# Kernel tuning notes

Measured on AMD Instinct MI355X. Metric: run time of the kernel, lower is better.

## Reference

```python
import jax, jax.numpy as jnp
import numpy as np

D = 1280      # embed_dim
H = 20        # num_heads
HD = D // H   # head_dim = 64
B = 4         # batch (number of requests)
ENC = 1500    # encoder length per request (Whisper 30s)
KV = B * ENC  # 6000 packed cross kv tokens
SEQ = [300, 500, 350, 450]  # ragged decoder lengths, sum = 1600
Q = sum(SEQ)


def setup_inputs() -> dict:
    key = jax.random.key(0)
    ks = jax.random.split(key, 8)
    s = 0.02
    return {
        "hidden_states": jax.random.normal(ks[0], (Q, D), jnp.float32),
        "cross_hidden_states": jax.random.normal(ks[1], (KV, D), jnp.float32),
        "seq_lens": jnp.array(SEQ, dtype=jnp.int32),
        "Wq": jax.random.normal(ks[2], (D, D), jnp.float32) * s,
        "bq": jax.random.normal(ks[3], (D,), jnp.float32) * s,
        "Wkv": jax.random.normal(ks[4], (D, 2 * D), jnp.float32) * s,
        "bkv": jax.random.normal(ks[5], (2 * D,), jnp.float32) * s,
        "Wo": jax.random.normal(ks[6], (D, D), jnp.float32) * s,
        "bo": jax.random.normal(ks[7], (D,), jnp.float32) * s,
    }


def reference(hidden_states, cross_hidden_states, seq_lens, Wq, bq, Wkv, bkv, Wo, bo):
    q_len, d = hidden_states.shape
    kv_len = cross_hidden_states.shape[0]
    bsz = seq_lens.shape[0]
    enc_len = kv_len // bsz
    scaling = jnp.float32(HD) ** -0.5

    # projections (packed tokens)
    q = (hidden_states @ Wq + bq) * scaling           # [Q, D]
    kv = cross_hidden_states @ Wkv + bkv              # [KV, 2D]
    k, v = kv[:, :d], kv[:, d:]

    # [H, L, HD]
    qh = q.reshape(q_len, H, HD).transpose(1, 0, 2)
    kh = k.reshape(kv_len, H, HD).transpose(1, 0, 2)
    vh = v.reshape(kv_len, H, HD).transpose(1, 0, 2)

    scores = jnp.einsum("hqd,hkd->hqk", qh, kh)       # [H, Q, KV]

    # ragged block-diagonal mask: query token i belongs to request
    # searchsorted(cumsum(seq_lens), i, 'right'); kv token j to j // enc_len
    cum = jnp.cumsum(seq_lens)
    q_req = jnp.searchsorted(cum, jnp.arange(q_len), side="right")
    kv_req = jnp.arange(kv_len) // enc_len
    mask = q_req[:, None] == kv_req[None, :]          # [Q, KV] bool

    scores = jnp.where(mask[None, :, :], scores, -jnp.inf)
    probs = jax.nn.softmax(scores, axis=-1)
    attn = jnp.einsum("hqk,hkd->hqd", probs, vh)      # [H, Q, HD]
    attn = attn.transpose(1, 0, 2).reshape(q_len, d)
    return attn @ Wo + bo
```

## Files before the change

### kernel.cpp

```cpp
#include <hip/hip_runtime.h>
#include <stdint.h>

#define AS1 __attribute__((address_space(1)))
#define AS3 __attribute__((address_space(3)))

typedef __bf16 bf16_t;
typedef bf16_t bf16x8 __attribute__((ext_vector_type(8)));
typedef float  f32x4  __attribute__((ext_vector_type(4)));
typedef float  f32x16 __attribute__((ext_vector_type(16)));
typedef unsigned short u16;

constexpr int D     = 1280;
constexpr int H     = 20;
constexpr int HD    = 64;
constexpr int NQ    = 1600;
constexpr int NKV   = 6000;
constexpr int ENC   = 1500;
constexpr int QPAD  = 1632;
constexpr int KVP   = 1504;
constexpr int KVTOT = 4 * KVP;
constexpr int KB_PER_REQ = KVP / 32;
constexpr int KB_TOT     = 4 * KB_PER_REQ;

__device__ __forceinline__ u16 f2bf(float f) {
  union { float f; uint32_t u; } x; x.f = f;
  uint32_t r = (x.u + 0x7fffu + ((x.u >> 16) & 1u)) >> 16;
  return (u16)r;
}

__device__ __forceinline__ void gload16(const void* g, void* l) {
  __builtin_amdgcn_global_load_lds((AS1 void*)g, (AS3 void*)l, 16, 0, 0);
}

__device__ __forceinline__ void cvt_body(const float* __restrict__ in, u16* __restrict__ out,
                                         int i, int n4) {
  if (i >= n4) return;
  float4 v = ((const float4*)in)[i];
  ushort4 o;
  o.x = f2bf(v.x); o.y = f2bf(v.y); o.z = f2bf(v.z); o.w = f2bf(v.w);
  ((ushort4*)out)[i] = o;
}

__device__ __forceinline__ void tpose_body(const float* __restrict__ in, u16* __restrict__ out,
                                           int R, int C, int bx, int by, u16 (*tile)[33]) {
  int bc = bx * 32, br = by * 32;
  int tx = threadIdx.x & 31, ty = threadIdx.x >> 5;
#pragma unroll
  for (int i = 0; i < 32; i += 8)
    tile[ty + i][tx] = f2bf(in[(size_t)(br + ty + i) * C + bc + tx]);
  __syncthreads();
#pragma unroll
  for (int i = 0; i < 32; i += 8)
    out[(size_t)(bc + ty + i) * R + br + tx] = tile[tx][ty + i];
}

__global__ __launch_bounds__(256)
void prep_kernel(const float* __restrict__ hs, const float* __restrict__ chs,
                 const float* __restrict__ Wq, const float* __restrict__ Wkv,
                 const float* __restrict__ Wo,
                 u16* __restrict__ hsb, u16* __restrict__ chsb,
                 u16* __restrict__ Wqt, u16* __restrict__ Wkvt, u16* __restrict__ Wot) {
  __shared__ u16 tile[32][33];
  int b = blockIdx.x;
  if (b < 2000) {
    cvt_body(hs, hsb, b * 256 + threadIdx.x, 512000);
  } else if (b < 9500) {
    cvt_body(chs, chsb, (b - 2000) * 256 + threadIdx.x, 1920000);
  } else if (b < 11100) {
    int t = b - 9500;  tpose_body(Wq,  Wqt,  1280, 1280, t % 40, t / 40, tile);
  } else if (b < 14300) {
    int t = b - 11100; tpose_body(Wkv, Wkvt, 1280, 2560, t % 80, t / 80, tile);
  } else {
    int t = b - 14300; tpose_body(Wo,  Wot,  1280, 1280, t % 40, t / 40, tile);
  }
}

template <int MODE>
__device__ __forceinline__ void gemm_tile(
    int m0, int n0, const u16* __restrict__ A, const u16* __restrict__ Bt,
    const float* __restrict__ bias, int M,
    u16* __restrict__ outA, u16* __restrict__ outB, float* __restrict__ outF,
    u16* As, u16* Bs) {
  const int tid = threadIdx.x;
  const int lane = tid & 63, l15 = lane & 15, lg = lane >> 4;
  const int w = tid >> 6, wr = w >> 1, wc = w & 1;

  const bool vside = (MODE == 1) && (n0 >= D);

  f32x4 acc[4][4] = {};

  for (int k0 = 0; k0 < D; k0 += 64) {
#pragma unroll
    for (int p = 0; p < 4; ++p) {
      int off = p * 4096 + tid * 16;
      int lg_off = off ^ (((off >> 7) & 7) << 4);
      int row = lg_off >> 7, kb = lg_off & 127;
      int gr = m0 + row; gr = gr < M ? gr : M - 1;
      gload16((const char*)A + ((size_t)gr * D + k0) * 2 + kb, (char*)As + off);
    }
#pragma unroll
    for (int p = 0; p < 4; ++p) {
      int off = p * 4096 + tid * 16;
      int lg_off = off ^ (((off >> 7) & 7) << 4);
      int row = lg_off >> 7, kb = lg_off & 127;
      int gr = n0 + row;
      gload16((const char*)Bt + ((size_t)gr * D + k0) * 2 + kb, (char*)Bs + off);
    }
    __syncthreads();
#pragma unroll
    for (int kk = 0; kk < 2; ++kk) {
      const int kbyte = kk * 64 + lg * 16;
      bf16x8 af[4], bfr[4];
#pragma unroll
      for (int m = 0; m < 4; ++m) {
        int row = wr * 64 + m * 16 + l15;
        int addr = ((row << 7) + kbyte) ^ ((row & 7) << 4);
        af[m] = *(const bf16x8*)((const char*)As + addr);
      }
#pragma unroll
      for (int n = 0; n < 4; ++n) {
        int row = wc * 64 + n * 16 + l15;
        int addr = ((row << 7) + kbyte) ^ ((row & 7) << 4);
        bfr[n] = *(const bf16x8*)((const char*)Bs + addr);
      }
      if (!vside) {
#pragma unroll
        for (int m = 0; m < 4; ++m)
#pragma unroll
          for (int n = 0; n < 4; ++n)
            acc[m][n] = __builtin_amdgcn_mfma_f32_16x16x32_bf16(af[m], bfr[n], acc[m][n], 0, 0, 0);
      } else {
#pragma unroll
        for (int m = 0; m < 4; ++m)
#pragma unroll
          for (int n = 0; n < 4; ++n)
            acc[m][n] = __builtin_amdgcn_mfma_f32_16x16x32_bf16(bfr[n], af[m], acc[m][n], 0, 0, 0);
      }
    }
    __syncthreads();
  }

  if (!vside) {
#pragma unroll
    for (int m = 0; m < 4; ++m)
#pragma unroll
      for (int n = 0; n < 4; ++n) {
        int col = n0 + wc * 64 + n * 16 + l15;
        float bv = bias[col];
#pragma unroll
        for (int r = 0; r < 4; ++r) {
          int row = m0 + wr * 64 + m * 16 + lg * 4 + r;
          if (row >= M) continue;
          float v = acc[m][n][r] + bv;
          if (MODE == 0) {
            v *= 0.125f;
            int h = col >> 6, hd = col & 63;
            outA[((size_t)(h * QPAD + row)) * HD + hd] = f2bf(v);
          } else {
            int req = row / ENC, loc = row - req * ENC;
            int rr = req * KVP + loc;
            int h = col >> 6, hd = col & 63;
            int kb2 = rr >> 5, kv = rr & 31;
            outA[((size_t)((h * KB_TOT + kb2) * 4 + (hd >> 4))) * 512 + kv * 16 + (hd & 15)] = f2bf(v);
          }
        }
      }
  } else {
    float bvv[4][4];
#pragma unroll
    for (int n = 0; n < 4; ++n)
#pragma unroll
      for (int r = 0; r < 4; ++r)
        bvv[n][r] = bias[n0 + wc * 64 + n * 16 + lg * 4 + r];
#pragma unroll
    for (int m = 0; m < 4; ++m) {
      int gm = m0 + wr * 64 + m * 16 + l15;
      int req = gm / ENC, loc = gm - req * ENC;
      int rr = req * KVP + loc;
      int kb2 = rr >> 5, kv = rr & 31;
      bool ok = gm < M;
#pragma unroll
      for (int n = 0; n < 4; ++n)
#pragma unroll
        for (int r = 0; r < 4; ++r) {
          if (!ok) continue;
          int c2 = n0 + wc * 64 + n * 16 + lg * 4 + r - D;
          int h = c2 >> 6, hd = c2 & 63;
          outB[((size_t)((h * KB_TOT + kb2) * 64 + hd)) * 32 + kv] = f2bf(acc[m][n][r] + bvv[n][r]);
        }
    }
  }
}

__global__ __launch_bounds__(256)
void qkv_gemm_kernel(const u16* __restrict__ hsb, const u16* __restrict__ chsb,
                     const u16* __restrict__ Wqt, const u16* __restrict__ Wkvt,
                     const float* __restrict__ bq, const float* __restrict__ bkv,
                     u16* __restrict__ qhb, u16* __restrict__ khb, u16* __restrict__ vtb) {
  __shared__ __align__(16) u16 As[128 * 64];
  __shared__ __align__(16) u16 Bs[128 * 64];
  const int bid = blockIdx.x;
  if (bid < 940) {
    const int q8 = 940 >> 3, r8 = 940 & 7;
    const int xcd = bid & 7, pos = bid >> 3;
    const int wg = (xcd < r8 ? xcd * (q8 + 1) : r8 * (q8 + 1) + (xcd - r8) * q8) + pos;
    gemm_tile<1>((wg / 20) * 128, (wg % 20) * 128, chsb, Wkvt, bkv, NKV,
                 khb, vtb, nullptr, As, Bs);
  } else {
    const int b2 = bid - 940;
    const int q8 = 130 >> 3, r8 = 130 & 7;
    const int xcd = b2 & 7, pos = b2 >> 3;
    const int wg = (xcd < r8 ? xcd * (q8 + 1) : r8 * (q8 + 1) + (xcd - r8) * q8) + pos;
    gemm_tile<0>((wg / 10) * 128, (wg % 10) * 128, hsb, Wqt, bq, NQ,
                 qhb, nullptr, nullptr, As, Bs);
  }
}

__global__ __launch_bounds__(256)
void o_gemm_kernel(const u16* __restrict__ attnb, const u16* __restrict__ Wot,
                   const float* __restrict__ bo, float* __restrict__ out) {
  __shared__ __align__(16) u16 As[128 * 64];
  __shared__ __align__(16) u16 Bs[64 * 64];
  const int nwg = 260, q8 = nwg >> 3, r8 = nwg & 7;
  const int xcd = blockIdx.x & 7, pos = blockIdx.x >> 3;
  const int wg = (xcd < r8 ? xcd * (q8 + 1) : r8 * (q8 + 1) + (xcd - r8) * q8) + pos;
  const int m0 = (wg / 20) * 128, n0 = (wg % 20) * 64;

  const int tid = threadIdx.x;
  const int lane = tid & 63, l15 = lane & 15, lg = lane >> 4;
  const int w = tid >> 6, wr = w >> 1, wc = w & 1;

  f32x4 acc[4][2] = {};

  for (int k0 = 0; k0 < D; k0 += 64) {
#pragma unroll
    for (int p = 0; p < 4; ++p) {
      int off = p * 4096 + tid * 16;
      int lg_off = off ^ (((off >> 7) & 7) << 4);
      int row = lg_off >> 7, kb = lg_off & 127;
      int gr = m0 + row; gr = gr < NQ ? gr : NQ - 1;
      gload16((const char*)attnb + ((size_t)gr * D + k0) * 2 + kb, (char*)As + off);
    }
#pragma unroll
    for (int p = 0; p < 2; ++p) {
      int off = p * 4096 + tid * 16;
      int lg_off = off ^ (((off >> 7) & 7) << 4);
      int row = lg_off >> 7, kb = lg_off & 127;
      gload16((const char*)Wot + ((size_t)(n0 + row) * D + k0) * 2 + kb, (char*)Bs + off);
    }
    __syncthreads();
#pragma unroll
    for (int kk = 0; kk < 2; ++kk) {
      const int kbyte = kk * 64 + lg * 16;
      bf16x8 af[4], bfr[2];
#pragma unroll
      for (int m = 0; m < 4; ++m) {
        int row = wr * 64 + m * 16 + l15;
        int addr = ((row << 7) + kbyte) ^ ((row & 7) << 4);
        af[m] = *(const bf16x8*)((const char*)As + addr);
      }
#pragma unroll
      for (int n = 0; n < 2; ++n) {
        int row = wc * 32 + n * 16 + l15;
        int addr = ((row << 7) + kbyte) ^ ((row & 7) << 4);
        bfr[n] = *(const bf16x8*)((const char*)Bs + addr);
      }
#pragma unroll
      for (int m = 0; m < 4; ++m)
#pragma unroll
        for (int n = 0; n < 2; ++n)
          acc[m][n] = __builtin_amdgcn_mfma_f32_16x16x32_bf16(af[m], bfr[n], acc[m][n], 0, 0, 0);
    }
    __syncthreads();
  }

#pragma unroll
  for (int m = 0; m < 4; ++m)
#pragma unroll
    for (int n = 0; n < 2; ++n) {
      int col = n0 + wc * 32 + n * 16 + l15;
      float bv = bo[col];
#pragma unroll
      for (int r = 0; r < 4; ++r) {
        int row = m0 + wr * 64 + m * 16 + lg * 4 + r;
        if (row >= NQ) continue;
        out[(size_t)row * D + col] = acc[m][n][r] + bv;
      }
    }
}

__global__ __launch_bounds__(256)
void attn_kernel(const u16* __restrict__ kbuf, const u16* __restrict__ vbuf,
                 const u16* __restrict__ qh, const int* __restrict__ seq,
                 u16* __restrict__ attnb) {
  __shared__ __align__(16) float smem[4][2176];
  const int lane = threadIdx.x & 63;
  const int l31 = lane & 31, h5 = lane >> 5;
  const int w = threadIdx.x >> 6;

  const int xcd = blockIdx.x & 7, pos = blockIdx.x >> 3;
  const int g = xcd * 160 + pos;
  const int p = g >> 4, t = g & 15;
  const int head = p >> 2, req = p & 3;

  int s0 = seq[0], s1 = seq[1], s2 = seq[2];
  int qstart = (req > 0 ? s0 : 0) + (req > 1 ? s1 : 0) + (req > 2 ? s2 : 0);
  int slen = seq[req];
  int q0 = t * 32;
  if (q0 >= slen) return;

  const u16* qrow = qh + ((size_t)(head * QPAD + qstart + q0 + l31)) * HD + h5 * 8;
  bf16x8 qb[4];
#pragma unroll
  for (int ks = 0; ks < 4; ++ks) qb[ks] = *(const bf16x8*)(qrow + ks * 16);

  const u16* kpan = kbuf + (size_t)(head * KB_TOT + req * KB_PER_REQ) * 2048 + l31 * 16 + h5 * 8;
  const u16* vpan = vbuf + (size_t)(head * KB_TOT + req * KB_PER_REQ) * 2048 + l31 * 32 + h5 * 8;
  const float C = 1.44269504088896340736f;
  const float KC = 16.0f * C;

  f32x16 o0 = {}, o1 = {};
  float ls = 0.f;

  const int kvs = w * 384;
  const int kve = (w == 3) ? ENC : kvs + 384;

  bf16x8 kA[4], vA[2][2], kB[4], vB[2][2];

  auto loadKV = [&](bf16x8 (&kk)[4], bf16x8 (&vv)[2][2], int blk) {
    const u16* kp = kpan + (size_t)blk * 2048;
    const u16* vp = vpan + (size_t)blk * 2048;
#pragma unroll
    for (int ks = 0; ks < 4; ++ks) kk[ks] = *(const bf16x8*)(kp + ks * 512);
#pragma unroll
    for (int dt = 0; dt < 2; ++dt)
#pragma unroll
      for (int ks = 0; ks < 2; ++ks)
        vv[dt][ks] = *(const bf16x8*)(vp + dt * 1024 + ks * 16);
  };

  auto step = [&](const bf16x8 (&kk)[4], const bf16x8 (&vv)[2][2], int kvb2, bool mask) {
    f32x16 sa = {};
    __builtin_amdgcn_s_setprio(1);
#pragma unroll
    for (int ks = 0; ks < 4; ++ks)
      sa = __builtin_amdgcn_mfma_f32_32x32x16_bf16(kk[ks], qb[ks], sa, 0, 0, 0);
    __builtin_amdgcn_s_setprio(0);

    if (mask) {
#pragma unroll
      for (int r = 0; r < 16; ++r) {
        int kvr = (r & 3) + 4 * h5 + 8 * (r >> 2);
        sa[r] = (kvb2 + kvr >= ENC) ? -__builtin_inff() : sa[r];
      }
    }

    float psum = 0.f;
#pragma unroll
    for (int r = 0; r < 16; ++r) { sa[r] = exp2f(fmaf(sa[r], C, -KC)); psum += sa[r]; }
    ls += psum;

    uint32_t a[8], x[8];
#pragma unroll
    for (int i = 0; i < 8; ++i) {
      union { bf16_t b[2]; uint32_t u; } tpk;
      tpk.b[0] = (bf16_t)sa[2 * i];
      tpk.b[1] = (bf16_t)sa[2 * i + 1];
      a[i] = tpk.u;
    }
#pragma unroll
    for (int i = 0; i < 8; ++i) x[i] = (uint32_t)__shfl_xor((int)a[i], 32);
    union { uint32_t w4[4]; bf16x8 v; } pb0, pb1;
    pb0.w4[0] = h5 ? x[2] : a[0]; pb0.w4[1] = h5 ? x[3] : a[1];
    pb0.w4[2] = h5 ? a[2] : x[0]; pb0.w4[3] = h5 ? a[3] : x[1];
    pb1.w4[0] = h5 ? x[6] : a[4]; pb1.w4[1] = h5 ? x[7] : a[5];
    pb1.w4[2] = h5 ? a[6] : x[4]; pb1.w4[3] = h5 ? a[7] : x[5];

    __builtin_amdgcn_s_setprio(1);
    o0 = __builtin_amdgcn_mfma_f32_32x32x16_bf16(vv[0][0], pb0.v, o0, 0, 0, 0);
    o0 = __builtin_amdgcn_mfma_f32_32x32x16_bf16(vv[0][1], pb1.v, o0, 0, 0, 0);
    o1 = __builtin_amdgcn_mfma_f32_32x32x16_bf16(vv[1][0], pb0.v, o1, 0, 0, 0);
    o1 = __builtin_amdgcn_mfma_f32_32x32x16_bf16(vv[1][1], pb1.v, o1, 0, 0, 0);
    __builtin_amdgcn_s_setprio(0);
  };

  loadKV(kA, vA, kvs >> 5);
  int kvb = kvs;
  while (kvb + 64 <= kve) {
    loadKV(kB, vB, (kvb + 32) >> 5);
    step(kA, vA, kvb, false);
    int nxt = kvb + 64;
    loadKV(kA, vA, (nxt < kve ? nxt : kvs) >> 5);
    step(kB, vB, kvb + 32, false);
    kvb += 64;
  }
  if (kvb < kve)
    step(kA, vA, kvb, true);

  ls += __shfl_xor(ls, 32);

#pragma unroll
  for (int r = 0; r < 16; ++r) {
    int drow = (r & 3) + 8 * (r >> 2) + 4 * h5;
    smem[w][drow * 33 + l31] = o0[r];
    smem[w][(drow + 32) * 33 + l31] = o1[r];
  }
  if (h5 == 0) smem[w][2144 + l31] = ls;
  __syncthreads();

#pragma unroll
  for (int it = 0; it < 8; ++it) {
    int item = threadIdx.x + it * 256;
    int q = item >> 6, d = item & 63;
    float L = smem[0][2144 + q] + smem[1][2144 + q] +
              smem[2][2144 + q] + smem[3][2144 + q];
    float O = smem[0][d * 33 + q] + smem[1][d * 33 + q] +
              smem[2][d * 33 + q] + smem[3][d * 33 + q];
    int qr = q0 + q;
    if (qr < slen)
      attnb[(size_t)(qstart + qr) * D + head * HD + d] = f2bf(O / L);
  }
}

extern "C" void kernel_launch(void* const* d_in, const int* in_sizes, int n_in,
                              void* d_out, int out_size, void* d_ws, size_t ws_size,
                              hipStream_t stream) {
  const float* hs  = (const float*)d_in[0];
  const float* chs = (const float*)d_in[1];
  const int*   seq = (const int*)d_in[2];
  const float* Wq  = (const float*)d_in[3];
  const float* bq  = (const float*)d_in[4];
  const float* Wkv = (const float*)d_in[5];
  const float* bkv = (const float*)d_in[6];
  const float* Wo  = (const float*)d_in[7];
  const float* bo  = (const float*)d_in[8];

  char* ws = (char*)d_ws;
  u16* hsb   = (u16*)(ws + 0);
  u16* chsb  = (u16*)(ws + 4096000);
  u16* Wqt   = (u16*)(ws + 19456000);
  u16* Wkvt  = (u16*)(ws + 22732800);
  u16* Wot   = (u16*)(ws + 29286400);
  u16* qhb   = (u16*)(ws + 32563200);
  u16* khb   = (u16*)(ws + 36741120);
  u16* vtb   = (u16*)(ws + 52142080);
  u16* attnb = (u16*)(ws + 67543040);

  prep_kernel<<<15900, 256, 0, stream>>>(hs, chs, Wq, Wkv, Wo, hsb, chsb, Wqt, Wkvt, Wot);
  qkv_gemm_kernel<<<1070, 256, 0, stream>>>(hsb, chsb, Wqt, Wkvt, bq, bkv, qhb, khb, vtb);
  attn_kernel<<<1280, 256, 0, stream>>>(khb, vtb, qhb, seq, attnb);
  o_gemm_kernel<<<260, 256, 0, stream>>>(attnb, Wot, bo, (float*)d_out);
}
```

Before: 157.4 us.

## Raise attention kernel occupancy by halving LDS and dropping register double-buffering

```diff
diff --git a/kernel.cpp b/kernel.cpp
--- a/kernel.cpp
+++ b/kernel.cpp
@@ -289,11 +289,11 @@
     }
 }
 
-__global__ __launch_bounds__(256)
+__global__ __launch_bounds__(256, 4)
 void attn_kernel(const u16* __restrict__ kbuf, const u16* __restrict__ vbuf,
                  const u16* __restrict__ qh, const int* __restrict__ seq,
                  u16* __restrict__ attnb) {
-  __shared__ __align__(16) float smem[4][2176];
+  __shared__ __align__(16) float smem[4][1088];
   const int lane = threadIdx.x & 63;
   const int l31 = lane & 31, h5 = lane >> 5;
   const int w = threadIdx.x >> 6;
@@ -325,11 +325,10 @@
   const int kvs = w * 384;
   const int kve = (w == 3) ? ENC : kvs + 384;
 
-  bf16x8 kA[4], vA[2][2], kB[4], vB[2][2];
-
-  auto loadKV = [&](bf16x8 (&kk)[4], bf16x8 (&vv)[2][2], int blk) {
-    const u16* kp = kpan + (size_t)blk * 2048;
-    const u16* vp = vpan + (size_t)blk * 2048;
+  auto step = [&](int kvb2, bool mask) {
+    const u16* kp = kpan + (size_t)(kvb2 >> 5) * 2048;
+    const u16* vp = vpan + (size_t)(kvb2 >> 5) * 2048;
+    bf16x8 kk[4], vv[2][2];
 #pragma unroll
     for (int ks = 0; ks < 4; ++ks) kk[ks] = *(const bf16x8*)(kp + ks * 512);
 #pragma unroll
@@ -337,9 +336,7 @@
 #pragma unroll
       for (int ks = 0; ks < 2; ++ks)
         vv[dt][ks] = *(const bf16x8*)(vp + dt * 1024 + ks * 16);
-  };
-
-  auto step = [&](const bf16x8 (&kk)[4], const bf16x8 (&vv)[2][2], int kvb2, bool mask) {
+
     f32x16 sa = {};
     __builtin_amdgcn_s_setprio(1);
 #pragma unroll
@@ -384,41 +381,35 @@
     __builtin_amdgcn_s_setprio(0);
   };
 
-  loadKV(kA, vA, kvs >> 5);
   int kvb = kvs;
-  while (kvb + 64 <= kve) {
-    loadKV(kB, vB, (kvb + 32) >> 5);
-    step(kA, vA, kvb, false);
-    int nxt = kvb + 64;
-    loadKV(kA, vA, (nxt < kve ? nxt : kvs) >> 5);
-    step(kB, vB, kvb + 32, false);
-    kvb += 64;
-  }
-  if (kvb < kve)
-    step(kA, vA, kvb, true);
+  for (; kvb + 32 <= kve; kvb += 32) step(kvb, false);
+  if (kvb < kve) step(kvb, true);
 
   ls += __shfl_xor(ls, 32);
 
 #pragma unroll
-  for (int r = 0; r < 16; ++r) {
-    int drow = (r & 3) + 8 * (r >> 2) + 4 * h5;
-    smem[w][drow * 33 + l31] = o0[r];
-    smem[w][(drow + 32) * 33 + l31] = o1[r];
-  }
-  if (h5 == 0) smem[w][2144 + l31] = ls;
-  __syncthreads();
-
-#pragma unroll
-  for (int it = 0; it < 8; ++it) {
-    int item = threadIdx.x + it * 256;
-    int q = item >> 6, d = item & 63;
-    float L = smem[0][2144 + q] + smem[1][2144 + q] +
-              smem[2][2144 + q] + smem[3][2144 + q];
-    float O = smem[0][d * 33 + q] + smem[1][d * 33 + q] +
-              smem[2][d * 33 + q] + smem[3][d * 33 + q];
-    int qr = q0 + q;
-    if (qr < slen)
-      attnb[(size_t)(qstart + qr) * D + head * HD + d] = f2bf(O / L);
+  for (int pass = 0; pass < 2; ++pass) {
+    if (pass) __syncthreads();
+#pragma unroll
+    for (int r = 0; r < 16; ++r) {
+      int drow = (r & 3) + 8 * (r >> 2) + 4 * h5;
+      smem[w][drow * 33 + l31] = pass ? o1[r] : o0[r];
+    }
+    if (pass == 0 && h5 == 0) smem[w][1056 + l31] = ls;
+    __syncthreads();
+
+#pragma unroll
+    for (int it = 0; it < 4; ++it) {
+      int item = threadIdx.x + it * 256;
+      int q = item >> 5, d = item & 31;
+      float L = smem[0][1056 + q] + smem[1][1056 + q] +
+                smem[2][1056 + q] + smem[3][1056 + q];
+      float O = smem[0][d * 33 + q] + smem[1][d * 33 + q] +
+                smem[2][d * 33 + q] + smem[3][d * 33 + q];
+      int qr = q0 + q;
+      if (qr < slen)
+        attnb[(size_t)(qstart + qr) * D + head * HD + pass * 32 + d] = f2bf(O / L);
+    }
   }
 }
 
```

Result: faster. 153.0 us (median of 2 runs) (-2.7%).
